# Kernel optimization log

Hardware: AMD Instinct MI355X
Metric: run time of the kernel (lower is better)

Reference implementation:

```python
import jax, jax.numpy as jnp
from jax import lax
import numpy as np

B, C, H, W = 16, 64, 256, 256
K = 3
PAD = (K - 1) // 2


def setup_inputs() -> dict:
    key = jax.random.key(0)
    ks = jax.random.split(key, 5)
    x = jax.random.normal(ks[0], (B, C, H, W), dtype=jnp.float32)
    # conv1: 1x1 conv dim -> dim*k*k, stored as a (C*K*K, C) matrix since input is (b,c,1,1)
    w1 = jax.random.normal(ks[1], (C * K * K, C), dtype=jnp.float32) * 0.1
    b1 = jax.random.normal(ks[2], (C * K * K,), dtype=jnp.float32) * 0.1
    fscale = jax.random.normal(ks[3], (C,), dtype=jnp.float32) * 0.1
    conv_bias = jax.random.normal(ks[4], (C,), dtype=jnp.float32) * 0.1
    return {"x": x, "w1": w1, "b1": b1, "fscale": fscale, "conv_bias": conv_bias}


def reference(x, w1, b1, fscale, conv_bias):
    b, c, h, w = x.shape
    # global average pool -> (b, c)
    avg = x.mean(axis=(2, 3))
    # 1x1 conv on (b,c,1,1) == dense matmul: (b, c*k*k)
    dyn = avg @ w1.T + b1
    # per-sample, per-channel depthwise kernels, sigmoid-gated
    wk = jax.nn.sigmoid(dyn).reshape(b * c, 1, K, K)  # (b*c, 1, k, k)
    # batch folded into channels -> grouped conv with feature_group_count = b*c
    xf = x.reshape(1, b * c, h, w)
    y = lax.conv_general_dilated(
        xf, wk,
        window_strides=(1, 1),
        padding=[(PAD, PAD), (PAD, PAD)],
        feature_group_count=b * c,
        dimension_numbers=("NCHW", "OIHW", "NCHW"),
    )
    y = y.reshape(b, c, h, w) + conv_bias[None, :, None, None]
    # gated residual blend: (x - y) * fscale * x + y
    fs = fscale[None, :, None, None]
    return (x - y) * fs * x + y
```

## Files before the change

kernel.cpp:

```cpp
#include <hip/hip_runtime.h>
#include <math.h>

#define BB 16
#define CC 64
#define HH 256
#define WW 256
#define HWSZ (HH * WW)
#define NP (BB * CC)
#define STRIPS 4
#define RPW (HH / (STRIPS * 4))

typedef float f4 __attribute__((ext_vector_type(4)));

__global__ __launch_bounds__(256) void mean_kernel(const float* __restrict__ x,
                                                   float* __restrict__ avg) {
    int p = blockIdx.x;
    const float4* xp = (const float4*)(x + (size_t)p * HWSZ);
    float s0 = 0.f, s1 = 0.f, s2 = 0.f, s3 = 0.f;
    for (int i = threadIdx.x; i < HWSZ / 4; i += 1024) {
        float4 a = xp[i];
        float4 b = xp[i + 256];
        float4 c = xp[i + 512];
        float4 d = xp[i + 768];
        s0 += a.x + a.y + a.z + a.w;
        s1 += b.x + b.y + b.z + b.w;
        s2 += c.x + c.y + c.z + c.w;
        s3 += d.x + d.y + d.z + d.w;
    }
    float s = (s0 + s1) + (s2 + s3);
    for (int off = 32; off > 0; off >>= 1) s += __shfl_down(s, off, 64);
    __shared__ float ws[4];
    int lane = threadIdx.x & 63, wid = threadIdx.x >> 6;
    if (lane == 0) ws[wid] = s;
    __syncthreads();
    if (threadIdx.x == 0) {
        avg[p] = (ws[0] + ws[1] + ws[2] + ws[3]) * (1.0f / (float)HWSZ);
    }
}

__global__ __launch_bounds__(256, 4) void conv_kernel(const float* __restrict__ x,
                                                      const float* __restrict__ avg,
                                                      const float* __restrict__ w1,
                                                      const float* __restrict__ b1,
                                                      const float* __restrict__ fscale,
                                                      const float* __restrict__ conv_bias,
                                                      float* __restrict__ out) {
    const int p     = (NP - 1) - (blockIdx.x >> 2);
    const int strip = blockIdx.x & (STRIPS - 1);
    const int wave  = threadIdx.x >> 6;
    const int lane  = threadIdx.x & 63;
    const int c = p & (CC - 1);
    const int b = p >> 6;
    const int h0 = strip * (HH / STRIPS) + wave * RPW;
    const float* xp = x + (size_t)p * HWSZ;
    float* op = out + (size_t)p * HWSZ;

    __shared__ float kk[12];
    if (threadIdx.x < 9) {
        const float* a    = avg + b * CC;
        const float* wrow = w1 + (size_t)(c * 9 + threadIdx.x) * CC;
        float s = b1[c * 9 + threadIdx.x];
#pragma unroll
        for (int c2 = 0; c2 < CC; ++c2) s += a[c2] * wrow[c2];
        kk[threadIdx.x] = 1.0f / (1.0f + expf(-s));
    }
    __syncthreads();
    const float k0 = kk[0], k1 = kk[1], k2 = kk[2];
    const float k3 = kk[3], k4 = kk[4], k5 = kk[5];
    const float k6 = kk[6], k7 = kk[7], k8 = kk[8];
    const float fs = fscale[c];
    const float cb = conv_bias[c];

    auto ldrow = [&](int r) -> f4 {
        if ((unsigned)r < (unsigned)HH) return ((const f4*)(xp + r * WW))[lane];
        return (f4){0.f, 0.f, 0.f, 0.f};
    };
    auto hL = [&](f4 v) { float t = __shfl_up(v.w, 1, 64); return lane == 0 ? 0.f : t; };
    auto hR = [&](f4 v) { float t = __shfl_down(v.x, 1, 64); return lane == 63 ? 0.f : t; };

    f4 rA = ldrow(h0 - 1);
    f4 rB = ldrow(h0);
    f4 rC = ldrow(h0 + 1);
    f4 rD = ldrow(h0 + 2);
    float lA = hL(rA), RA = hR(rA);
    float lB = hL(rB), RB = hR(rB);
    float lC = hL(rC), RC = hR(rC);
    float lD = hL(rD), RD = hR(rD);

    for (int h = h0; h < h0 + RPW; h += 2) {
        f4 rE = ldrow(h + 3);
        f4 rF = ldrow(h + 4);

        f4 y0;
        y0.x = cb + k0 * lA   + k1 * rA.x + k2 * rA.y
                  + k3 * lB   + k4 * rB.x + k5 * rB.y
                  + k6 * lC   + k7 * rC.x + k8 * rC.y;
        y0.y = cb + k0 * rA.x + k1 * rA.y + k2 * rA.z
                  + k3 * rB.x + k4 * rB.y + k5 * rB.z
                  + k6 * rC.x + k7 * rC.y + k8 * rC.z;
        y0.z = cb + k0 * rA.y + k1 * rA.z + k2 * rA.w
                  + k3 * rB.y + k4 * rB.z + k5 * rB.w
                  + k6 * rC.y + k7 * rC.z + k8 * rC.w;
        y0.w = cb + k0 * rA.z + k1 * rA.w + k2 * RA
                  + k3 * rB.z + k4 * rB.w + k5 * RB
                  + k6 * rC.z + k7 * rC.w + k8 * RC;
        f4 o0;
        o0.x = (rB.x - y0.x) * fs * rB.x + y0.x;
        o0.y = (rB.y - y0.y) * fs * rB.y + y0.y;
        o0.z = (rB.z - y0.z) * fs * rB.z + y0.z;
        o0.w = (rB.w - y0.w) * fs * rB.w + y0.w;
        __builtin_nontemporal_store(o0, (f4*)(op + h * WW) + lane);

        f4 y1;
        y1.x = cb + k0 * lB   + k1 * rB.x + k2 * rB.y
                  + k3 * lC   + k4 * rC.x + k5 * rC.y
                  + k6 * lD   + k7 * rD.x + k8 * rD.y;
        y1.y = cb + k0 * rB.x + k1 * rB.y + k2 * rB.z
                  + k3 * rC.x + k4 * rC.y + k5 * rC.z
                  + k6 * rD.x + k7 * rD.y + k8 * rD.z;
        y1.z = cb + k0 * rB.y + k1 * rB.z + k2 * rB.w
                  + k3 * rC.y + k4 * rC.z + k5 * rC.w
                  + k6 * rD.y + k7 * rD.z + k8 * rD.w;
        y1.w = cb + k0 * rB.z + k1 * rB.w + k2 * RB
                  + k3 * rC.z + k4 * rC.w + k5 * RC
                  + k6 * rD.z + k7 * rD.w + k8 * RD;
        f4 o1;
        o1.x = (rC.x - y1.x) * fs * rC.x + y1.x;
        o1.y = (rC.y - y1.y) * fs * rC.y + y1.y;
        o1.z = (rC.z - y1.z) * fs * rC.z + y1.z;
        o1.w = (rC.w - y1.w) * fs * rC.w + y1.w;
        __builtin_nontemporal_store(o1, (f4*)(op + (h + 1) * WW) + lane);

        float lE = hL(rE), RE = hR(rE);
        float lF = hL(rF), RF = hR(rF);

        rA = rC; lA = lC; RA = RC;
        rB = rD; lB = lD; RB = RD;
        rC = rE; lC = lE; RC = RE;
        rD = rF; lD = lF; RD = RF;
    }
}

extern "C" void kernel_launch(void* const* d_in, const int* in_sizes, int n_in,
                              void* d_out, int out_size, void* d_ws, size_t ws_size,
                              hipStream_t stream) {
    const float* x         = (const float*)d_in[0];
    const float* w1        = (const float*)d_in[1];
    const float* b1        = (const float*)d_in[2];
    const float* fscale    = (const float*)d_in[3];
    const float* conv_bias = (const float*)d_in[4];
    float* out = (float*)d_out;

    float* avg = (float*)d_ws;

    mean_kernel<<<NP, 256, 0, stream>>>(x, avg);
    conv_kernel<<<NP * STRIPS, 256, 0, stream>>>(x, avg, w1, b1, fscale, conv_bias, out);
}
```

Measured before the change: 488.2 us.

## Process batch in groups so conv re-reads input from last-level cache

Splits the batch into four groups and runs the mean and conv kernels per group, so each group's input (about 64MB) can stay resident in the large last-level cache between the reduction pass and the convolution pass. The mean kernel is also split into quarter-plane blocks for more parallelism, with the partial sums combined when the dynamic weights are computed. The cost is more kernel launches and a tail/drain at each group boundary.

```diff
diff --git a/kernel.cpp b/kernel.cpp
--- a/kernel.cpp
+++ b/kernel.cpp
@@ -7,21 +7,26 @@
 #define WW 256
 #define HWSZ (HH * WW)
 #define NP (BB * CC)
+#define GROUPS 4
+#define BPG (BB / GROUPS)
+#define PPG (BPG * CC)
+#define QROWS (HH / 4)
 #define STRIPS 4
 #define RPW (HH / (STRIPS * 4))
 
 typedef float f4 __attribute__((ext_vector_type(4)));
 
-__global__ __launch_bounds__(256) void mean_kernel(const float* __restrict__ x,
-                                                   float* __restrict__ avg) {
-    int p = blockIdx.x;
-    const float4* xp = (const float4*)(x + (size_t)p * HWSZ);
+__global__ __launch_bounds__(256) void mean_kernel(const float* __restrict__ xg,
+                                                   float* __restrict__ avg4g) {
+    const int pl = blockIdx.x >> 2;
+    const int q  = blockIdx.x & 3;
+    const f4* xv = (const f4*)(xg + (size_t)pl * HWSZ + (size_t)q * QROWS * WW);
     float s0 = 0.f, s1 = 0.f, s2 = 0.f, s3 = 0.f;
-    for (int i = threadIdx.x; i < HWSZ / 4; i += 1024) {
-        float4 a = xp[i];
-        float4 b = xp[i + 256];
-        float4 c = xp[i + 512];
-        float4 d = xp[i + 768];
+    for (int i = threadIdx.x; i < 1024; i += 256) {
+        f4 a = xv[i];
+        f4 b = xv[i + 1024];
+        f4 c = xv[i + 2048];
+        f4 d = xv[i + 3072];
         s0 += a.x + a.y + a.z + a.w;
         s1 += b.x + b.y + b.z + b.w;
         s2 += c.x + c.y + c.z + c.w;
@@ -34,34 +39,38 @@
     if (lane == 0) ws[wid] = s;
     __syncthreads();
     if (threadIdx.x == 0) {
-        avg[p] = (ws[0] + ws[1] + ws[2] + ws[3]) * (1.0f / (float)HWSZ);
+        avg4g[pl * 4 + q] = ws[0] + ws[1] + ws[2] + ws[3];
     }
 }
 
-__global__ __launch_bounds__(256, 4) void conv_kernel(const float* __restrict__ x,
-                                                      const float* __restrict__ avg,
+__global__ __launch_bounds__(256, 4) void conv_kernel(const float* __restrict__ xg,
+                                                      const float* __restrict__ avg4g,
                                                       const float* __restrict__ w1,
                                                       const float* __restrict__ b1,
                                                       const float* __restrict__ fscale,
                                                       const float* __restrict__ conv_bias,
-                                                      float* __restrict__ out) {
-    const int p     = (NP - 1) - (blockIdx.x >> 2);
+                                                      float* __restrict__ outg) {
+    const int pl    = blockIdx.x >> 2;
     const int strip = blockIdx.x & (STRIPS - 1);
     const int wave  = threadIdx.x >> 6;
     const int lane  = threadIdx.x & 63;
-    const int c = p & (CC - 1);
-    const int b = p >> 6;
+    const int c  = pl & (CC - 1);
+    const int bl = pl >> 6;
     const int h0 = strip * (HH / STRIPS) + wave * RPW;
-    const float* xp = x + (size_t)p * HWSZ;
-    float* op = out + (size_t)p * HWSZ;
+    const float* xp = xg + (size_t)pl * HWSZ;
+    float* op = outg + (size_t)pl * HWSZ;
 
     __shared__ float kk[12];
     if (threadIdx.x < 9) {
-        const float* a    = avg + b * CC;
+        const float* a4   = avg4g + (size_t)bl * CC * 4;
         const float* wrow = w1 + (size_t)(c * 9 + threadIdx.x) * CC;
         float s = b1[c * 9 + threadIdx.x];
 #pragma unroll
-        for (int c2 = 0; c2 < CC; ++c2) s += a[c2] * wrow[c2];
+        for (int c2 = 0; c2 < CC; ++c2) {
+            float av = (a4[c2 * 4 + 0] + a4[c2 * 4 + 1] +
+                        a4[c2 * 4 + 2] + a4[c2 * 4 + 3]) * (1.0f / (float)HWSZ);
+            s += av * wrow[c2];
+        }
         kk[threadIdx.x] = 1.0f / (1.0f + expf(-s));
     }
     __syncthreads();
@@ -150,9 +159,14 @@
     const float* fscale    = (const float*)d_in[3];
     const float* conv_bias = (const float*)d_in[4];
     float* out = (float*)d_out;
+    float* avg4 = (float*)d_ws;
 
-    float* avg = (float*)d_ws;
-
-    mean_kernel<<<NP, 256, 0, stream>>>(x, avg);
-    conv_kernel<<<NP * STRIPS, 256, 0, stream>>>(x, avg, w1, b1, fscale, conv_bias, out);
+    for (int g = 0; g < GROUPS; ++g) {
+        const float* xg     = x    + (size_t)g * PPG * HWSZ;
+        float*       outg   = out  + (size_t)g * PPG * HWSZ;
+        float*       avg4g  = avg4 + (size_t)g * PPG * 4;
+        mean_kernel<<<PPG * 4, 256, 0, stream>>>(xg, avg4g);
+        conv_kernel<<<PPG * STRIPS, 256, 0, stream>>>(xg, avg4g, w1, b1,
+                                                      fscale, conv_bias, outg);
+    }
 }
```

New measurement: 505.8 us. 1.04x slower.
